# Kernel optimization log

Hardware: AMD Instinct MI355X
Metric: run time of the kernel (lower is better)

The kernel has to match this reference:

```python
import jax, jax.numpy as jnp
import numpy as np

B, C, H, W = 8, 128, 64, 64


def setup_inputs() -> dict:
    key = jax.random.key(0)
    ks = jax.random.split(key, 9)
    d = C
    return {
        "x": jax.random.normal(ks[0], (B, C, H, W), dtype=jnp.float32),
        "qw": jax.random.normal(ks[1], (d, d), dtype=jnp.float32),
        "qb": jax.random.normal(ks[2], (d,), dtype=jnp.float32),
        "kw": jax.random.normal(ks[3], (d, d), dtype=jnp.float32),
        "kb": jax.random.normal(ks[4], (d,), dtype=jnp.float32),
        "vw": jax.random.normal(ks[5], (d, d), dtype=jnp.float32),
        "vb": jax.random.normal(ks[6], (d,), dtype=jnp.float32),
        "proj_w": jax.random.normal(ks[7], (d, d), dtype=jnp.float32),
        "proj_b": jax.random.normal(ks[8], (d,), dtype=jnp.float32),
    }


def reference(x, qw, qb, kw, kb, vw, vb, proj_w, proj_b):
    b, c, h, w = x.shape
    n = h * w  # number of spatial tokens
    # permute to channels-last and flatten spatial dims: (b, n, c)
    xt = jnp.transpose(x, (0, 2, 3, 1)).reshape(b, n, c)
    q = xt @ qw + qb
    k = xt @ kw + kb
    v = xt @ vw + vb
    scale = c ** (-0.5)
    # full (n x n) attention over flattened spatial tokens, single head
    attn = jax.nn.softmax(jnp.einsum("bnc,bmc->bnm", q, k) * scale, axis=-1)
    hout = jnp.einsum("bnm,bmc->bnc", attn, v) @ proj_w + proj_b
    out = xt + hout  # residual is on the permuted (channels-last) x, per source
    return out.reshape(b, h, w, c)
```

## Files before the change

kernel.cpp:

```cpp
#include <hip/hip_runtime.h>

#define NB 8
#define CD 128
#define NN 4096
#define SCALE 0.08838834764831845f
#define L2E 1.44269504088896f
#define QSCALE (SCALE * L2E)

typedef __bf16 bf16x8 __attribute__((ext_vector_type(8)));
typedef float f32x4 __attribute__((ext_vector_type(4)));

__device__ __forceinline__ unsigned swz256(unsigned row, unsigned b) {
  unsigned s = b >> 4, o = b & 15u;
  unsigned sw = (s & 8u) | ((s & 7u) ^ (row & 7u));
  return row * 256u + sw * 16u + o;
}
__device__ __forceinline__ unsigned swz128(unsigned row, unsigned b) {
  unsigned s = b >> 4, o = b & 15u;
  unsigned sw = (s ^ row) & 7u;
  return row * 128u + sw * 16u + o;
}
__device__ __forceinline__ unsigned swzP(unsigned row, unsigned b) {
  unsigned s = b >> 4, o = b & 15u;
  unsigned sw = (s ^ (row ^ (row >> 2))) & 7u;
  return row * 128u + sw * 16u + o;
}

#define DPP_ROR_F(x, N)                                                       \
  __builtin_bit_cast(float, __builtin_amdgcn_update_dpp(                      \
      __builtin_bit_cast(int, (x)), __builtin_bit_cast(int, (x)),             \
      0x120 + (N), 0xF, 0xF, false))

__global__ __launch_bounds__(256, 2) void qkv_kernel(
    const float* __restrict__ x,
    const float* __restrict__ qw, const float* __restrict__ qb,
    const float* __restrict__ kw, const float* __restrict__ kb,
    const float* __restrict__ vw, const float* __restrict__ vb,
    __bf16* __restrict__ Qh, __bf16* __restrict__ Ql,
    __bf16* __restrict__ Kh, __bf16* __restrict__ Kl,
    __bf16* __restrict__ Vt)
{
  __shared__ __align__(16) unsigned char sm[49664];
  const int tid = threadIdx.x;
  const int lane = tid & 63, wv = tid >> 6;
  const int l15 = lane & 15, g = lane >> 4;
  const int b = blockIdx.x & 7;
  const int n0 = (blockIdx.x >> 3) * 64;
  const f32x4 Z4 = {0.f, 0.f, 0.f, 0.f};

  #pragma unroll 4
  for (int i = 0; i < 32; ++i) {
    int e = i * 256 + tid;
    int nl = e & 63, c = e >> 6;
    float f = x[((size_t)(b * CD + c)) * NN + n0 + nl];
    __bf16 h = (__bf16)f;
    __bf16 lo = (__bf16)(f - (float)h);
    unsigned off = swz256((unsigned)nl, (unsigned)(c * 2));
    *(__bf16*)(sm + off) = h;
    *(__bf16*)(sm + 16384 + off) = lo;
  }
  __syncthreads();

  bf16x8 ah[4], al[4];
  #pragma unroll
  for (int kk = 0; kk < 4; ++kk) {
    unsigned off = swz256((unsigned)(wv * 16 + l15), (unsigned)(kk * 64 + g * 16));
    ah[kk] = *(const bf16x8*)(sm + off);
    al[kk] = *(const bf16x8*)(sm + 16384 + off);
  }

  for (int mat = 0; mat < 2; ++mat) {
    const float* gw = mat ? kw : qw;
    const float* gb = mat ? kb : qb;
    __bf16* Oh = mat ? Kh : Qh;
    __bf16* Ol = mat ? Kl : Ql;
    const float sc = mat ? 1.0f : QSCALE;
    for (int qd = 0; qd < 4; ++qd) {
      #pragma unroll 4
      for (int i = 0; i < 16; ++i) {
        int e = i * 256 + tid;
        int dl = e & 31, c = e >> 5;
        float f = gw[c * CD + qd * 32 + dl];
        __bf16 h = (__bf16)f;
        __bf16 lo = (__bf16)(f - (float)h);
        unsigned off = swz256((unsigned)dl, (unsigned)(c * 2));
        *(__bf16*)(sm + 32768 + off) = h;
        *(__bf16*)(sm + 40960 + off) = lo;
      }
      __syncthreads();
      #pragma unroll
      for (int fr = 0; fr < 2; ++fr) {
        f32x4 acc = Z4;
        #pragma unroll
        for (int kk = 0; kk < 4; ++kk) {
          unsigned off = swz256((unsigned)(fr * 16 + l15), (unsigned)(kk * 64 + g * 16));
          bf16x8 bh = *(const bf16x8*)(sm + 32768 + off);
          bf16x8 bl = *(const bf16x8*)(sm + 40960 + off);
          acc = __builtin_amdgcn_mfma_f32_16x16x32_bf16(ah[kk], bh, acc, 0, 0, 0);
          acc = __builtin_amdgcn_mfma_f32_16x16x32_bf16(ah[kk], bl, acc, 0, 0, 0);
          acc = __builtin_amdgcn_mfma_f32_16x16x32_bf16(al[kk], bh, acc, 0, 0, 0);
        }
        const int dout = qd * 32 + fr * 16 + l15;
        const float bias = gb[dout];
        #pragma unroll
        for (int r = 0; r < 4; ++r) {
          int row = n0 + wv * 16 + g * 4 + r;
          float v = (acc[r] + bias) * sc;
          __bf16 h = (__bf16)v;
          __bf16 lo = (__bf16)(v - (float)h);
          size_t go = ((size_t)(b * NN + row)) * CD + dout;
          Oh[go] = h;
          Ol[go] = lo;
        }
      }
      __syncthreads();
    }
  }

  f32x4 accV[8];
  #pragma unroll
  for (int i = 0; i < 8; ++i) accV[i] = Z4;
  for (int qd = 0; qd < 4; ++qd) {
    #pragma unroll 4
    for (int i = 0; i < 16; ++i) {
      int e = i * 256 + tid;
      int dl = e & 31, c = e >> 5;
      float f = vw[c * CD + qd * 32 + dl];
      *(__bf16*)(sm + 32768 + swz256((unsigned)dl, (unsigned)(c * 2))) = (__bf16)f;
    }
    __syncthreads();
    #pragma unroll
    for (int fr = 0; fr < 2; ++fr) {
      f32x4 acc = accV[qd * 2 + fr];
      #pragma unroll
      for (int kk = 0; kk < 4; ++kk) {
        unsigned off = swz256((unsigned)(fr * 16 + l15), (unsigned)(kk * 64 + g * 16));
        bf16x8 bh = *(const bf16x8*)(sm + 32768 + off);
        acc = __builtin_amdgcn_mfma_f32_16x16x32_bf16(ah[kk], bh, acc, 0, 0, 0);
      }
      accV[qd * 2 + fr] = acc;
    }
    __syncthreads();
  }
  #pragma unroll
  for (int df = 0; df < 8; ++df) {
    int dout = df * 16 + l15;
    float bias = vb[dout];
    #pragma unroll
    for (int r = 0; r < 4; ++r) {
      int row = wv * 16 + g * 4 + r;
      *(__bf16*)(sm + 32768 + (row * 132 + dout) * 2) = (__bf16)(accV[df][r] + bias);
    }
  }
  __syncthreads();
  #pragma unroll 4
  for (int i = 0; i < 32; ++i) {
    int e = i * 256 + tid;
    int nl = e & 63, dout = e >> 6;
    __bf16 v = *(const __bf16*)(sm + 32768 + (nl * 132 + dout) * 2);
    Vt[((size_t)(b * CD + dout)) * NN + n0 + nl] = v;
  }
}

__global__ __launch_bounds__(256, 2) void attn_kernel(
    const __bf16* __restrict__ Qh, const __bf16* __restrict__ Ql,
    const __bf16* __restrict__ Kh, const __bf16* __restrict__ Kl,
    const __bf16* __restrict__ Vt, const float* __restrict__ x,
    const float* __restrict__ pw, const float* __restrict__ pb,
    float* __restrict__ out)
{
  __shared__ __align__(16) unsigned char sm[57344];
  const int tid = threadIdx.x;
  const int lane = tid & 63, wv = tid >> 6;
  const int l15 = lane & 15, g = lane >> 4;
  const int b = blockIdx.x & 7;
  const int q0 = (blockIdx.x >> 3) * 64;
  const f32x4 Z4 = {0.f, 0.f, 0.f, 0.f};

  bf16x8 qh[4], ql[4];
  #pragma unroll
  for (int kk = 0; kk < 4; ++kk) {
    size_t off = ((size_t)(b * NN + q0 + wv * 16 + l15)) * CD + kk * 32 + g * 8;
    qh[kk] = *(const bf16x8*)(Qh + off);
    ql[kk] = *(const bf16x8*)(Ql + off);
  }

  bf16x8 bones;
  {
    __bf16 v = (l15 == 0) ? (__bf16)1.0f : (__bf16)0.0f;
    #pragma unroll
    for (int j = 0; j < 8; ++j) bones[j] = v;
  }

  f32x4 accO[8];
  #pragma unroll
  for (int i = 0; i < 8; ++i) accO[i] = Z4;
  f32x4 accL = Z4;
  float mrow[4];
  #pragma unroll
  for (int r = 0; r < 4; ++r) mrow[r] = -__builtin_inff();

  bf16x8 pkh[4], pkl[4], pvv[4];
  const int rK = tid >> 4, sK = tid & 15;
  const int rV = tid >> 3, sV = tid & 7;

  #define ISSUE_TILE(KT)                                                        \
    {                                                                           \
      const size_t kb_ = (size_t)(b * NN + (KT) * 64);                          \
      _Pragma("unroll")                                                         \
      for (int i = 0; i < 4; ++i) {                                             \
        pkh[i] = *(const bf16x8*)(Kh + (kb_ + i * 16 + rK) * CD + sK * 8);      \
        pkl[i] = *(const bf16x8*)(Kl + (kb_ + i * 16 + rK) * CD + sK * 8);      \
        pvv[i] = *(const bf16x8*)(Vt + ((size_t)(b * CD) + i * 32 + rV) * NN +  \
                                  (KT) * 64 + sV * 8);                          \
      }                                                                         \
    }
  #define COMMIT_TILE()                                                         \
    {                                                                           \
      _Pragma("unroll")                                                         \
      for (int i = 0; i < 4; ++i) {                                             \
        unsigned o_ = swz256((unsigned)(i * 16 + rK), (unsigned)(sK * 16));     \
        *(bf16x8*)(sm + o_) = pkh[i];                                           \
        *(bf16x8*)(sm + 16384 + o_) = pkl[i];                                   \
        *(bf16x8*)(sm + 32768 +                                                 \
                   swz128((unsigned)(i * 32 + rV), (unsigned)(sV * 16))) = pvv[i]; \
      }                                                                         \
    }

  ISSUE_TILE(0);
  COMMIT_TILE();
  __syncthreads();

  for (int kt = 0; kt < 64; ++kt) {
    if (kt < 63) ISSUE_TILE(kt + 1);
    __builtin_amdgcn_sched_barrier(0);

    f32x4 s4[4];
    #pragma unroll
    for (int kf = 0; kf < 4; ++kf) s4[kf] = Z4;
    __builtin_amdgcn_s_setprio(1);
    #pragma unroll
    for (int kf = 0; kf < 4; ++kf) {
      #pragma unroll
      for (int kk = 0; kk < 4; ++kk) {
        unsigned off = swz256((unsigned)(kf * 16 + l15), (unsigned)(kk * 64 + g * 16));
        bf16x8 bh = *(const bf16x8*)(sm + off);
        bf16x8 bl = *(const bf16x8*)(sm + 16384 + off);
        s4[kf] = __builtin_amdgcn_mfma_f32_16x16x32_bf16(qh[kk], bh, s4[kf], 0, 0, 0);
        s4[kf] = __builtin_amdgcn_mfma_f32_16x16x32_bf16(qh[kk], bl, s4[kf], 0, 0, 0);
        s4[kf] = __builtin_amdgcn_mfma_f32_16x16x32_bf16(ql[kk], bh, s4[kf], 0, 0, 0);
      }
    }
    __builtin_amdgcn_s_setprio(0);

    float mnew[4];
    bool grow = false;
    #pragma unroll
    for (int r = 0; r < 4; ++r) {
      float mx = fmaxf(fmaxf(s4[0][r], s4[1][r]), fmaxf(s4[2][r], s4[3][r]));
      mx = fmaxf(mx, DPP_ROR_F(mx, 8));
      mx = fmaxf(mx, DPP_ROR_F(mx, 4));
      mx = fmaxf(mx, DPP_ROR_F(mx, 2));
      mx = fmaxf(mx, DPP_ROR_F(mx, 1));
      float mn = fmaxf(mrow[r], mx);
      mnew[r] = mn;
      grow = grow || (mn > mrow[r]);
      #pragma unroll
      for (int kf = 0; kf < 4; ++kf)
        s4[kf][r] = exp2f(s4[kf][r] - mn);
    }
    if (__any((int)grow)) {
      #pragma unroll
      for (int r = 0; r < 4; ++r) {
        float alpha = exp2f(mrow[r] - mnew[r]);
        accL[r] *= alpha;
        #pragma unroll
        for (int df = 0; df < 8; ++df) accO[df][r] *= alpha;
      }
    }
    #pragma unroll
    for (int r = 0; r < 4; ++r) mrow[r] = mnew[r];

    #pragma unroll
    for (int kf = 0; kf < 4; ++kf) {
      #pragma unroll
      for (int r = 0; r < 4; ++r) {
        unsigned row = (unsigned)(wv * 16 + g * 4 + r);
        *(__bf16*)(sm + 49152 + swzP(row, (unsigned)((kf * 16 + l15) * 2))) =
            (__bf16)s4[kf][r];
      }
    }

    bf16x8 pa[2];
    #pragma unroll
    for (int kk2 = 0; kk2 < 2; ++kk2)
      pa[kk2] = *(const bf16x8*)(sm + 49152 +
                  swzP((unsigned)(wv * 16 + l15), (unsigned)(kk2 * 64 + g * 16)));
    __builtin_amdgcn_s_setprio(1);
    accL = __builtin_amdgcn_mfma_f32_16x16x32_bf16(pa[0], bones, accL, 0, 0, 0);
    accL = __builtin_amdgcn_mfma_f32_16x16x32_bf16(pa[1], bones, accL, 0, 0, 0);
    #pragma unroll
    for (int df = 0; df < 8; ++df) {
      #pragma unroll
      for (int kk2 = 0; kk2 < 2; ++kk2) {
        bf16x8 bv = *(const bf16x8*)(sm + 32768 +
                      swz128((unsigned)(df * 16 + l15), (unsigned)(kk2 * 64 + g * 16)));
        accO[df] = __builtin_amdgcn_mfma_f32_16x16x32_bf16(pa[kk2], bv, accO[df], 0, 0, 0);
      }
    }
    __builtin_amdgcn_s_setprio(0);

    __syncthreads();
    if (kt < 63) COMMIT_TILE();
    __syncthreads();
  }
  #undef ISSUE_TILE
  #undef COMMIT_TILE

  float rl[4];
  #pragma unroll
  for (int r = 0; r < 4; ++r) {
    float lv = __shfl(accL[r], lane & 48);
    rl[r] = 1.0f / lv;
  }
  #pragma unroll
  for (int df = 0; df < 8; ++df) {
    #pragma unroll
    for (int r = 0; r < 4; ++r) {
      unsigned row = (unsigned)(wv * 16 + g * 4 + r);
      *(__bf16*)(sm + swz256(row, (unsigned)((df * 16 + l15) * 2))) =
          (__bf16)(accO[df][r] * rl[r]);
    }
  }
  #pragma unroll 4
  for (int i = 0; i < 16; ++i) {
    int e = i * 256 + tid;
    int c = e >> 5, d4 = e & 31;
    const float4 w4 = *(const float4*)(pw + c * CD + d4 * 4);
    *(__bf16*)(sm + 16384 + swz256((unsigned)(d4 * 4 + 0), (unsigned)(c * 2))) = (__bf16)w4.x;
    *(__bf16*)(sm + 16384 + swz256((unsigned)(d4 * 4 + 1), (unsigned)(c * 2))) = (__bf16)w4.y;
    *(__bf16*)(sm + 16384 + swz256((unsigned)(d4 * 4 + 2), (unsigned)(c * 2))) = (__bf16)w4.z;
    *(__bf16*)(sm + 16384 + swz256((unsigned)(d4 * 4 + 3), (unsigned)(c * 2))) = (__bf16)w4.w;
  }
  __syncthreads();

  bf16x8 oa[4];
  #pragma unroll
  for (int kk = 0; kk < 4; ++kk)
    oa[kk] = *(const bf16x8*)(sm + swz256((unsigned)(wv * 16 + l15),
                                          (unsigned)(kk * 64 + g * 16)));
  #pragma unroll
  for (int df = 0; df < 8; ++df) {
    f32x4 acc = Z4;
    #pragma unroll
    for (int kk = 0; kk < 4; ++kk) {
      bf16x8 bw = *(const bf16x8*)(sm + 16384 +
                    swz256((unsigned)(df * 16 + l15), (unsigned)(kk * 64 + g * 16)));
      acc = __builtin_amdgcn_mfma_f32_16x16x32_bf16(oa[kk], bw, acc, 0, 0, 0);
    }
    const int cc = df * 16 + l15;
    const float bias = pb[cc];
    #pragma unroll
    for (int r = 0; r < 4; ++r) {
      int row = q0 + wv * 16 + g * 4 + r;
      float val = acc[r] + bias + x[((size_t)(b * CD + cc)) * NN + row];
      out[((size_t)(b * NN + row)) * CD + cc] = val;
    }
  }
}

extern "C" void kernel_launch(void* const* d_in, const int* in_sizes, int n_in,
                              void* d_out, int out_size, void* d_ws, size_t ws_size,
                              hipStream_t stream) {
  (void)in_sizes; (void)n_in; (void)out_size; (void)ws_size;
  const float* x  = (const float*)d_in[0];
  const float* qw = (const float*)d_in[1];
  const float* qb = (const float*)d_in[2];
  const float* kw = (const float*)d_in[3];
  const float* kb = (const float*)d_in[4];
  const float* vw = (const float*)d_in[5];
  const float* vb = (const float*)d_in[6];
  const float* pw = (const float*)d_in[7];
  const float* pb = (const float*)d_in[8];
  float* out = (float*)d_out;

  const size_t SZ = (size_t)NB * NN * CD;
  __bf16* Qh = (__bf16*)d_ws;
  __bf16* Ql = Qh + SZ;
  __bf16* Kh = Ql + SZ;
  __bf16* Kl = Kh + SZ;
  __bf16* Vt = Kl + SZ;

  dim3 grid(512), blk(256);
  qkv_kernel<<<grid, blk, 0, stream>>>(x, qw, qb, kw, kb, vw, vb,
                                       Qh, Ql, Kh, Kl, Vt);
  attn_kernel<<<grid, blk, 0, stream>>>(Qh, Ql, Kh, Kl, Vt, x, pw, pb, out);
}
```

Before: 300.4 us.

## Double-buffer K/V tiles via direct global-to-LDS loads with smaller key tiles

```diff
diff --git a/kernel.cpp b/kernel.cpp
--- a/kernel.cpp
+++ b/kernel.cpp
@@ -3,6 +3,7 @@
 #define NB 8
 #define CD 128
 #define NN 4096
+#define KV 32
 #define SCALE 0.08838834764831845f
 #define L2E 1.44269504088896f
 #define QSCALE (SCALE * L2E)
@@ -15,21 +16,22 @@
   unsigned sw = (s & 8u) | ((s & 7u) ^ (row & 7u));
   return row * 256u + sw * 16u + o;
 }
-__device__ __forceinline__ unsigned swz128(unsigned row, unsigned b) {
+__device__ __forceinline__ unsigned swz64(unsigned row, unsigned b) {
   unsigned s = b >> 4, o = b & 15u;
-  unsigned sw = (s ^ row) & 7u;
-  return row * 128u + sw * 16u + o;
-}
-__device__ __forceinline__ unsigned swzP(unsigned row, unsigned b) {
-  unsigned s = b >> 4, o = b & 15u;
-  unsigned sw = (s ^ (row ^ (row >> 2))) & 7u;
-  return row * 128u + sw * 16u + o;
+  unsigned sw = (s ^ (row >> 1)) & 3u;
+  return row * 64u + sw * 16u + o;
 }
 
 #define DPP_ROR_F(x, N)                                                       \
   __builtin_bit_cast(float, __builtin_amdgcn_update_dpp(                      \
       __builtin_bit_cast(int, (x)), __builtin_bit_cast(int, (x)),             \
       0x120 + (N), 0xF, 0xF, false))
+
+__device__ __forceinline__ void gload16(const __bf16* g, unsigned char* l) {
+  __builtin_amdgcn_global_load_lds(
+      (const __attribute__((address_space(1))) void*)g,
+      (__attribute__((address_space(3))) void*)l, 16, 0, 0);
+}
 
 __global__ __launch_bounds__(256, 2) void qkv_kernel(
     const float* __restrict__ x,
@@ -162,14 +164,14 @@
   }
 }
 
-__global__ __launch_bounds__(256, 2) void attn_kernel(
+__global__ __launch_bounds__(256, 3) void attn_kernel(
     const __bf16* __restrict__ Qh, const __bf16* __restrict__ Ql,
     const __bf16* __restrict__ Kh, const __bf16* __restrict__ Kl,
     const __bf16* __restrict__ Vt, const float* __restrict__ x,
     const float* __restrict__ pw, const float* __restrict__ pb,
     float* __restrict__ out)
 {
-  __shared__ __align__(16) unsigned char sm[57344];
+  __shared__ __align__(16) unsigned char sm[53248];
   const int tid = threadIdx.x;
   const int lane = tid & 63, wv = tid >> 6;
   const int l15 = lane & 15, g = lane >> 4;
@@ -200,50 +202,43 @@
   #pragma unroll
   for (int r = 0; r < 4; ++r) mrow[r] = -__builtin_inff();
 
-  bf16x8 pkh[4], pkl[4], pvv[4];
-  const int rK = tid >> 4, sK = tid & 15;
-  const int rV = tid >> 3, sV = tid & 7;
-
-  #define ISSUE_TILE(KT)                                                        \
-    {                                                                           \
-      const size_t kb_ = (size_t)(b * NN + (KT) * 64);                          \
-      _Pragma("unroll")                                                         \
-      for (int i = 0; i < 4; ++i) {                                             \
-        pkh[i] = *(const bf16x8*)(Kh + (kb_ + i * 16 + rK) * CD + sK * 8);      \
-        pkl[i] = *(const bf16x8*)(Kl + (kb_ + i * 16 + rK) * CD + sK * 8);      \
-        pvv[i] = *(const bf16x8*)(Vt + ((size_t)(b * CD) + i * 32 + rV) * NN +  \
-                                  (KT) * 64 + sV * 8);                          \
-      }                                                                         \
-    }
-  #define COMMIT_TILE()                                                         \
-    {                                                                           \
-      _Pragma("unroll")                                                         \
-      for (int i = 0; i < 4; ++i) {                                             \
-        unsigned o_ = swz256((unsigned)(i * 16 + rK), (unsigned)(sK * 16));     \
-        *(bf16x8*)(sm + o_) = pkh[i];                                           \
-        *(bf16x8*)(sm + 16384 + o_) = pkl[i];                                   \
-        *(bf16x8*)(sm + 32768 +                                                 \
-                   swz128((unsigned)(i * 32 + rV), (unsigned)(sV * 16))) = pvv[i]; \
-      }                                                                         \
-    }
-
-  ISSUE_TILE(0);
-  COMMIT_TILE();
+  #define ISSUE(KT, BUF)                                                       \
+    {                                                                          \
+      const int kb_ = b * NN + (KT) * KV;                                      \
+      _Pragma("unroll")                                                        \
+      for (int i = 0; i < 2; ++i) {                                            \
+        int rowK = wv * 8 + i * 4 + (lane >> 4);                               \
+        int sw16 = lane & 15;                                                  \
+        int sK_ = (sw16 & 8) | ((sw16 & 7) ^ (rowK & 7));                      \
+        gload16(Kh + (size_t)(kb_ + rowK) * CD + sK_ * 8,                      \
+                sm + (BUF) * 8192 + (wv * 8 + i * 4) * 256);                   \
+        gload16(Kl + (size_t)(kb_ + rowK) * CD + sK_ * 8,                      \
+                sm + 16384 + (BUF) * 8192 + (wv * 8 + i * 4) * 256);           \
+        int rowV = (wv * 2 + i) * 16 + (lane >> 2);                            \
+        int sV_ = ((lane & 3) ^ (rowV >> 1)) & 3;                              \
+        gload16(Vt + ((size_t)(b * CD) + rowV) * NN + (KT) * KV + sV_ * 8,     \
+                sm + 32768 + (BUF) * 8192 + ((wv * 2 + i) * 16) * 64);         \
+      }                                                                        \
+    }
+
+  ISSUE(0, 0);
   __syncthreads();
 
-  for (int kt = 0; kt < 64; ++kt) {
-    if (kt < 63) ISSUE_TILE(kt + 1);
+  for (int kt = 0; kt < 128; ++kt) {
+    const int cur = kt & 1;
+    if (kt < 127) ISSUE(kt + 1, cur ^ 1);
     __builtin_amdgcn_sched_barrier(0);
 
-    f32x4 s4[4];
-    #pragma unroll
-    for (int kf = 0; kf < 4; ++kf) s4[kf] = Z4;
+    f32x4 s4[2];
+    #pragma unroll
+    for (int kf = 0; kf < 2; ++kf) s4[kf] = Z4;
     __builtin_amdgcn_s_setprio(1);
     #pragma unroll
-    for (int kf = 0; kf < 4; ++kf) {
+    for (int kf = 0; kf < 2; ++kf) {
       #pragma unroll
       for (int kk = 0; kk < 4; ++kk) {
-        unsigned off = swz256((unsigned)(kf * 16 + l15), (unsigned)(kk * 64 + g * 16));
+        unsigned off = (unsigned)(cur * 8192) +
+                       swz256((unsigned)(kf * 16 + l15), (unsigned)(kk * 64 + g * 16));
         bf16x8 bh = *(const bf16x8*)(sm + off);
         bf16x8 bl = *(const bf16x8*)(sm + 16384 + off);
         s4[kf] = __builtin_amdgcn_mfma_f32_16x16x32_bf16(qh[kk], bh, s4[kf], 0, 0, 0);
@@ -257,7 +252,7 @@
     bool grow = false;
     #pragma unroll
     for (int r = 0; r < 4; ++r) {
-      float mx = fmaxf(fmaxf(s4[0][r], s4[1][r]), fmaxf(s4[2][r], s4[3][r]));
+      float mx = fmaxf(s4[0][r], s4[1][r]);
       mx = fmaxf(mx, DPP_ROR_F(mx, 8));
       mx = fmaxf(mx, DPP_ROR_F(mx, 4));
       mx = fmaxf(mx, DPP_ROR_F(mx, 2));
@@ -266,7 +261,7 @@
       mnew[r] = mn;
       grow = grow || (mn > mrow[r]);
       #pragma unroll
-      for (int kf = 0; kf < 4; ++kf)
+      for (int kf = 0; kf < 2; ++kf)
         s4[kf][r] = exp2f(s4[kf][r] - mn);
     }
     if (__any((int)grow)) {
@@ -282,40 +277,30 @@
     for (int r = 0; r < 4; ++r) mrow[r] = mnew[r];
 
     #pragma unroll
-    for (int kf = 0; kf < 4; ++kf) {
+    for (int kf = 0; kf < 2; ++kf) {
       #pragma unroll
       for (int r = 0; r < 4; ++r) {
         unsigned row = (unsigned)(wv * 16 + g * 4 + r);
-        *(__bf16*)(sm + 49152 + swzP(row, (unsigned)((kf * 16 + l15) * 2))) =
+        *(__bf16*)(sm + 49152 + swz64(row, (unsigned)((kf * 16 + l15) * 2))) =
             (__bf16)s4[kf][r];
       }
     }
 
-    bf16x8 pa[2];
-    #pragma unroll
-    for (int kk2 = 0; kk2 < 2; ++kk2)
-      pa[kk2] = *(const bf16x8*)(sm + 49152 +
-                  swzP((unsigned)(wv * 16 + l15), (unsigned)(kk2 * 64 + g * 16)));
+    bf16x8 pa = *(const bf16x8*)(sm + 49152 +
+                  swz64((unsigned)(wv * 16 + l15), (unsigned)(g * 16)));
     __builtin_amdgcn_s_setprio(1);
-    accL = __builtin_amdgcn_mfma_f32_16x16x32_bf16(pa[0], bones, accL, 0, 0, 0);
-    accL = __builtin_amdgcn_mfma_f32_16x16x32_bf16(pa[1], bones, accL, 0, 0, 0);
+    accL = __builtin_amdgcn_mfma_f32_16x16x32_bf16(pa, bones, accL, 0, 0, 0);
     #pragma unroll
     for (int df = 0; df < 8; ++df) {
-      #pragma unroll
-      for (int kk2 = 0; kk2 < 2; ++kk2) {
-        bf16x8 bv = *(const bf16x8*)(sm + 32768 +
-                      swz128((unsigned)(df * 16 + l15), (unsigned)(kk2 * 64 + g * 16)));
-        accO[df] = __builtin_amdgcn_mfma_f32_16x16x32_bf16(pa[kk2], bv, accO[df], 0, 0, 0);
-      }
+      bf16x8 bv = *(const bf16x8*)(sm + 32768 + cur * 8192 +
+                    swz64((unsigned)(df * 16 + l15), (unsigned)(g * 16)));
+      accO[df] = __builtin_amdgcn_mfma_f32_16x16x32_bf16(pa, bv, accO[df], 0, 0, 0);
     }
     __builtin_amdgcn_s_setprio(0);
 
     __syncthreads();
-    if (kt < 63) COMMIT_TILE();
-    __syncthreads();
-  }
-  #undef ISSUE_TILE
-  #undef COMMIT_TILE
+  }
+  #undef ISSUE
 
   float rl[4];
   #pragma unroll
```

New measurement: 315.1 us. 1.05x slower.

## Transpose QK^T MFMA and pass P through bpermute instead of shared memory

Applied to the files above, without the earlier changes.

```diff
diff --git a/kernel.cpp b/kernel.cpp
--- a/kernel.cpp
+++ b/kernel.cpp
@@ -3,6 +3,7 @@
 #define NB 8
 #define CD 128
 #define NN 4096
+#define KV 64
 #define SCALE 0.08838834764831845f
 #define L2E 1.44269504088896f
 #define QSCALE (SCALE * L2E)
@@ -20,16 +21,12 @@
   unsigned sw = (s ^ row) & 7u;
   return row * 128u + sw * 16u + o;
 }
-__device__ __forceinline__ unsigned swzP(unsigned row, unsigned b) {
-  unsigned s = b >> 4, o = b & 15u;
-  unsigned sw = (s ^ (row ^ (row >> 2))) & 7u;
-  return row * 128u + sw * 16u + o;
-}
-
-#define DPP_ROR_F(x, N)                                                       \
-  __builtin_bit_cast(float, __builtin_amdgcn_update_dpp(                      \
-      __builtin_bit_cast(int, (x)), __builtin_bit_cast(int, (x)),             \
-      0x120 + (N), 0xF, 0xF, false))
+
+__device__ __forceinline__ int cvt_pk_bf16(float lo, float hi) {
+  int w;
+  asm("v_cvt_pk_bf16_f32 %0, %1, %2" : "=v"(w) : "v"(lo), "v"(hi));
+  return w;
+}
 
 __global__ __launch_bounds__(256, 2) void qkv_kernel(
     const float* __restrict__ x,
@@ -169,7 +166,7 @@
     const float* __restrict__ pw, const float* __restrict__ pb,
     float* __restrict__ out)
 {
-  __shared__ __align__(16) unsigned char sm[57344];
+  __shared__ __align__(16) unsigned char sm[49152];
   const int tid = threadIdx.x;
   const int lane = tid & 63, wv = tid >> 6;
   const int l15 = lane & 15, g = lane >> 4;
@@ -196,43 +193,53 @@
   #pragma unroll
   for (int i = 0; i < 8; ++i) accO[i] = Z4;
   f32x4 accL = Z4;
-  float mrow[4];
-  #pragma unroll
-  for (int r = 0; r < 4; ++r) mrow[r] = -__builtin_inff();
+  float mrow = -__builtin_inff();
 
   bf16x8 pkh[4], pkl[4], pvv[4];
   const int rK = tid >> 4, sK = tid & 15;
   const int rV = tid >> 3, sV = tid & 7;
-
-  #define ISSUE_TILE(KT)                                                        \
-    {                                                                           \
-      const size_t kb_ = (size_t)(b * NN + (KT) * 64);                          \
-      _Pragma("unroll")                                                         \
-      for (int i = 0; i < 4; ++i) {                                             \
-        pkh[i] = *(const bf16x8*)(Kh + (kb_ + i * 16 + rK) * CD + sK * 8);      \
-        pkl[i] = *(const bf16x8*)(Kl + (kb_ + i * 16 + rK) * CD + sK * 8);      \
-        pvv[i] = *(const bf16x8*)(Vt + ((size_t)(b * CD) + i * 32 + rV) * NN +  \
-                                  (KT) * 64 + sV * 8);                          \
-      }                                                                         \
-    }
-  #define COMMIT_TILE()                                                         \
-    {                                                                           \
-      _Pragma("unroll")                                                         \
-      for (int i = 0; i < 4; ++i) {                                             \
-        unsigned o_ = swz256((unsigned)(i * 16 + rK), (unsigned)(sK * 16));     \
-        *(bf16x8*)(sm + o_) = pkh[i];                                           \
-        *(bf16x8*)(sm + 16384 + o_) = pkl[i];                                   \
-        *(bf16x8*)(sm + 32768 +                                                 \
+  const __bf16* bKh = Kh + (size_t)(b * NN) * CD;
+  const __bf16* bKl = Kl + (size_t)(b * NN) * CD;
+  const __bf16* bVt = Vt + (size_t)(b * CD) * NN;
+  int offK[4], offV[4];
+  #pragma unroll
+  for (int i = 0; i < 4; ++i) {
+    offK[i] = (i * 16 + rK) * CD + sK * 8;
+    offV[i] = (i * 32 + rV) * NN + sV * 8;
+  }
+  const int baseAddr = ((g & 1) * 32 + l15) * 4;
+  const int addrA = (g * 4) * 4;
+
+  #define ISSUE(KTOFFK, KTOFFV)                                                \
+    {                                                                          \
+      _Pragma("unroll")                                                        \
+      for (int i = 0; i < 4; ++i) {                                            \
+        pkh[i] = *(const bf16x8*)(bKh + (KTOFFK) + offK[i]);                   \
+        pkl[i] = *(const bf16x8*)(bKl + (KTOFFK) + offK[i]);                   \
+        pvv[i] = *(const bf16x8*)(bVt + (KTOFFV) + offV[i]);                   \
+      }                                                                        \
+    }
+  #define COMMIT()                                                             \
+    {                                                                          \
+      _Pragma("unroll")                                                        \
+      for (int i = 0; i < 4; ++i) {                                            \
+        unsigned o_ = swz256((unsigned)(i * 16 + rK), (unsigned)(sK * 16));    \
+        *(bf16x8*)(sm + o_) = pkh[i];                                          \
+        *(bf16x8*)(sm + 16384 + o_) = pkl[i];                                  \
+        *(bf16x8*)(sm + 32768 +                                                \
                    swz128((unsigned)(i * 32 + rV), (unsigned)(sV * 16))) = pvv[i]; \
-      }                                                                         \
-    }
-
-  ISSUE_TILE(0);
-  COMMIT_TILE();
+      }                                                                        \
+    }
+
+  ISSUE(0, 0);
+  COMMIT();
   __syncthreads();
 
+  int ktoffK = KV * CD, ktoffV = KV;
   for (int kt = 0; kt < 64; ++kt) {
-    if (kt < 63) ISSUE_TILE(kt + 1);
+    if (kt < 63) ISSUE(ktoffK, ktoffV);
+    ktoffK += KV * CD;
+    ktoffV += KV;
     __builtin_amdgcn_sched_barrier(0);
 
     f32x4 s4[4];
@@ -246,56 +253,65 @@
         unsigned off = swz256((unsigned)(kf * 16 + l15), (unsigned)(kk * 64 + g * 16));
         bf16x8 bh = *(const bf16x8*)(sm + off);
         bf16x8 bl = *(const bf16x8*)(sm + 16384 + off);
-        s4[kf] = __builtin_amdgcn_mfma_f32_16x16x32_bf16(qh[kk], bh, s4[kf], 0, 0, 0);
-        s4[kf] = __builtin_amdgcn_mfma_f32_16x16x32_bf16(qh[kk], bl, s4[kf], 0, 0, 0);
-        s4[kf] = __builtin_amdgcn_mfma_f32_16x16x32_bf16(ql[kk], bh, s4[kf], 0, 0, 0);
+        s4[kf] = __builtin_amdgcn_mfma_f32_16x16x32_bf16(bh, qh[kk], s4[kf], 0, 0, 0);
+        s4[kf] = __builtin_amdgcn_mfma_f32_16x16x32_bf16(bl, qh[kk], s4[kf], 0, 0, 0);
+        s4[kf] = __builtin_amdgcn_mfma_f32_16x16x32_bf16(bh, ql[kk], s4[kf], 0, 0, 0);
       }
     }
     __builtin_amdgcn_s_setprio(0);
 
-    float mnew[4];
-    bool grow = false;
-    #pragma unroll
-    for (int r = 0; r < 4; ++r) {
-      float mx = fmaxf(fmaxf(s4[0][r], s4[1][r]), fmaxf(s4[2][r], s4[3][r]));
-      mx = fmaxf(mx, DPP_ROR_F(mx, 8));
-      mx = fmaxf(mx, DPP_ROR_F(mx, 4));
-      mx = fmaxf(mx, DPP_ROR_F(mx, 2));
-      mx = fmaxf(mx, DPP_ROR_F(mx, 1));
-      float mn = fmaxf(mrow[r], mx);
-      mnew[r] = mn;
-      grow = grow || (mn > mrow[r]);
-      #pragma unroll
-      for (int kf = 0; kf < 4; ++kf)
-        s4[kf][r] = exp2f(s4[kf][r] - mn);
+    float mx = fmaxf(fmaxf(s4[0][0], s4[0][1]), fmaxf(s4[0][2], s4[0][3]));
+    #pragma unroll
+    for (int kf = 1; kf < 4; ++kf) {
+      mx = fmaxf(mx, fmaxf(fmaxf(s4[kf][0], s4[kf][1]),
+                           fmaxf(s4[kf][2], s4[kf][3])));
+    }
+    mx = fmaxf(mx, __shfl_xor(mx, 16));
+    mx = fmaxf(mx, __shfl_xor(mx, 32));
+    const float mn = fmaxf(mrow, mx);
+    const bool grow = mn > mrow;
+    #pragma unroll
+    for (int kf = 0; kf < 4; ++kf) {
+      #pragma unroll
+      for (int r = 0; r < 4; ++r) s4[kf][r] = exp2f(s4[kf][r] - mn);
     }
     if (__any((int)grow)) {
+      float alpha = exp2f(mrow - mn);
+      int aw = __builtin_bit_cast(int, alpha);
       #pragma unroll
       for (int r = 0; r < 4; ++r) {
-        float alpha = exp2f(mrow[r] - mnew[r]);
-        accL[r] *= alpha;
+        float ar = __builtin_bit_cast(float,
+                     __builtin_amdgcn_ds_bpermute(addrA + r * 4, aw));
+        accL[r] *= ar;
         #pragma unroll
-        for (int df = 0; df < 8; ++df) accO[df][r] *= alpha;
-      }
-    }
-    #pragma unroll
-    for (int r = 0; r < 4; ++r) mrow[r] = mnew[r];
-
+        for (int df = 0; df < 8; ++df) accO[df][r] *= ar;
+      }
+    }
+    mrow = mn;
+
+    int c01[4], c23[4];
     #pragma unroll
     for (int kf = 0; kf < 4; ++kf) {
-      #pragma unroll
-      for (int r = 0; r < 4; ++r) {
-        unsigned row = (unsigned)(wv * 16 + g * 4 + r);
-        *(__bf16*)(sm + 49152 + swzP(row, (unsigned)((kf * 16 + l15) * 2))) =
-            (__bf16)s4[kf][r];
-      }
-    }
-
+      c01[kf] = cvt_pk_bf16(s4[kf][0], s4[kf][1]);
+      c23[kf] = cvt_pk_bf16(s4[kf][2], s4[kf][3]);
+    }
     bf16x8 pa[2];
     #pragma unroll
-    for (int kk2 = 0; kk2 < 2; ++kk2)
-      pa[kk2] = *(const bf16x8*)(sm + 49152 +
-                  swzP((unsigned)(wv * 16 + l15), (unsigned)(kk2 * 64 + g * 16)));
+    for (int kk2 = 0; kk2 < 2; ++kk2) {
+      int w[4];
+      #pragma unroll
+      for (int wi = 0; wi < 4; ++wi) {
+        int se = (wi & 1) ? c23[kk2 * 2] : c01[kk2 * 2];
+        int so = (wi & 1) ? c23[kk2 * 2 + 1] : c01[kk2 * 2 + 1];
+        int a = baseAddr + (wi >> 1) * 64;
+        int ve = __builtin_amdgcn_ds_bpermute(a, se);
+        int vo = __builtin_amdgcn_ds_bpermute(a, so);
+        w[wi] = (g < 2) ? ve : vo;
+      }
+      int4 wv4 = {w[0], w[1], w[2], w[3]};
+      pa[kk2] = __builtin_bit_cast(bf16x8, wv4);
+    }
+
     __builtin_amdgcn_s_setprio(1);
     accL = __builtin_amdgcn_mfma_f32_16x16x32_bf16(pa[0], bones, accL, 0, 0, 0);
     accL = __builtin_amdgcn_mfma_f32_16x16x32_bf16(pa[1], bones, accL, 0, 0, 0);
@@ -311,11 +327,11 @@
     __builtin_amdgcn_s_setprio(0);
 
     __syncthreads();
-    if (kt < 63) COMMIT_TILE();
+    if (kt < 63) COMMIT();
     __syncthreads();
   }
-  #undef ISSUE_TILE
-  #undef COMMIT_TILE
+  #undef ISSUE
+  #undef COMMIT
 
   float rl[4];
   #pragma unroll
```

Result: no change. 297.5 us (-1.0%).
